# Performance work log

Measured on AMD Instinct MI355X. Metric: run time of the kernel, lower is better.

## Reference

```python
import jax, jax.numpy as jnp
import numpy as np

N, C, OUT, E, H = 4096, 256, 256, 131072, 8
DH = C // H
EPS = 1e-5


def layer_norm(h, g, b):
    mu = jnp.mean(h, axis=-1, keepdims=True)
    var = jnp.mean(jnp.square(h - mu), axis=-1, keepdims=True)
    return (h - mu) * jax.lax.rsqrt(var + EPS) * g + b


def setup_inputs() -> dict:
    key = jax.random.key(0)
    ks = jax.random.split(key, 12)
    s = 1.0 / np.sqrt(C)
    return {
        "x": jax.random.normal(ks[0], (N, C), jnp.float32),
        "edge_index": jax.random.randint(ks[1], (2, E), 0, N, jnp.int32),
        "edge_attr": jax.random.normal(ks[2], (E, C), jnp.float32),
        # nn.MultiheadAttention params
        "in_proj_w": jax.random.uniform(ks[3], (3 * C, C), jnp.float32, -s, s),
        "in_proj_b": jnp.zeros((3 * C,), jnp.float32),
        "attn_out_w": jax.random.uniform(ks[4], (C, C), jnp.float32, -s, s),
        "attn_out_b": jnp.zeros((C,), jnp.float32),
        # edge_mlp: Linear(3C -> OUT) + LayerNorm(OUT)
        "edge_w": jax.random.uniform(ks[5], (OUT, 3 * C), jnp.float32, -1 / np.sqrt(3 * C), 1 / np.sqrt(3 * C)),
        "edge_b": jax.random.uniform(ks[6], (OUT,), jnp.float32, -1 / np.sqrt(3 * C), 1 / np.sqrt(3 * C)),
        "ln1_g": jnp.ones((OUT,), jnp.float32),
        "ln1_b": jnp.zeros((OUT,), jnp.float32),
        # output_proj: Linear(C + OUT -> OUT)
        "out_w": jax.random.uniform(ks[7], (OUT, C + OUT), jnp.float32, -1 / np.sqrt(C + OUT), 1 / np.sqrt(C + OUT)),
        "out_b": jax.random.uniform(ks[8], (OUT,), jnp.float32, -1 / np.sqrt(C + OUT), 1 / np.sqrt(C + OUT)),
        "ln2_g": jnp.ones((OUT,), jnp.float32),
        "ln2_b": jnp.zeros((OUT,), jnp.float32),
    }


def reference(x, edge_index, edge_attr, in_proj_w, in_proj_b, attn_out_w, attn_out_b,
              edge_w, edge_b, ln1_g, ln1_b, out_w, out_b, ln2_g, ln2_b):
    num_nodes = x.shape[0]
    # --- dense self-attention over all nodes (seq len = N, batch 1) ---
    qkv = x @ in_proj_w.T + in_proj_b            # [N, 3C]
    q, k, v = jnp.split(qkv, 3, axis=-1)
    q = q.reshape(num_nodes, H, DH).transpose(1, 0, 2)  # [H, N, DH]
    k = k.reshape(num_nodes, H, DH).transpose(1, 0, 2)
    v = v.reshape(num_nodes, H, DH).transpose(1, 0, 2)
    scores = jnp.einsum("hqd,hkd->hqk", q, k) / np.sqrt(DH)
    attn = jax.nn.softmax(scores, axis=-1)       # dropout inactive at eval
    ctx = jnp.einsum("hqk,hkd->hqd", attn, v)    # [H, N, DH]
    ctx = ctx.transpose(1, 0, 2).reshape(num_nodes, C)
    x_attn = ctx @ attn_out_w.T + attn_out_b     # [N, C]
    # --- vectorized edge messages: gather -> MLP -> scatter-add ---
    row, col = edge_index[0], edge_index[1]
    msg_in = jnp.concatenate([x[row], x[col], edge_attr], axis=-1)  # [E, 3C]
    msg = jax.nn.relu(layer_norm(msg_in @ edge_w.T + edge_b, ln1_g, ln1_b))
    node_messages = jax.ops.segment_sum(msg, col, num_segments=num_nodes)  # [N, OUT]
    # --- combine, project, residual, norm ---
    combined = jnp.concatenate([x_attn, node_messages], axis=-1)
    out = combined @ out_w.T + out_b
    out = out + x                                # OUT == C so residual fires
    return layer_norm(out, ln2_g, ln2_b)
```

## Files before the change

### kernel.cpp

```cpp
#include <hip/hip_runtime.h>
#include <hip/hip_bf16.h>
#include <math.h>

typedef __bf16 bf16;
typedef __bf16 bf16x8 __attribute__((ext_vector_type(8)));
typedef __bf16 bf16x4 __attribute__((ext_vector_type(4)));
typedef float f32x4 __attribute__((ext_vector_type(4)));
typedef float f32x16 __attribute__((ext_vector_type(16)));

#define MFMA16(a, b, c) __builtin_amdgcn_mfma_f32_16x16x32_bf16((a), (b), (c), 0, 0, 0)
#define MFMA32(a, b, c) __builtin_amdgcn_mfma_f32_32x32x16_bf16((a), (b), (c), 0, 0, 0)

#define N_NODES 4096
#define C_DIM   256
#define E_EDGES 131072
#define APAD    280
#define TPAD    260

__device__ __forceinline__ float ldf(const void* p, int i, bool f32) {
    return f32 ? ((const float*)p)[i] : (float)((const bf16*)p)[i];
}

__device__ __forceinline__ bf16x8 ld8(const void* base, size_t off, bool f32) {
    if (f32) {
        const float* p = (const float*)base + off;
        float4 a = *(const float4*)p;
        float4 b = *(const float4*)(p + 4);
        bf16x8 r;
        r[0] = (bf16)a.x; r[1] = (bf16)a.y; r[2] = (bf16)a.z; r[3] = (bf16)a.w;
        r[4] = (bf16)b.x; r[5] = (bf16)b.y; r[6] = (bf16)b.z; r[7] = (bf16)b.w;
        return r;
    }
    return *(const bf16x8*)((const bf16*)base + off);
}

__device__ __forceinline__ unsigned cvtpk(float a, float b) {
    unsigned r;
    asm("v_cvt_pk_bf16_f32 %0, %1, %2" : "=v"(r) : "v"(a), "v"(b));
    return r;
}
__device__ __forceinline__ void pl32swap(unsigned &a, unsigned &b) {
    asm volatile("v_permlane32_swap_b32 %0, %1" : "+v"(a), "+v"(b));
}

union PW { unsigned u[4]; bf16x8 v; };

__global__ __launch_bounds__(64) void detect_dtype(const void* x, int* flag)
{
    const bf16* xb = (const bf16*)x;
    int tid = threadIdx.x;
    int bad = 0;
    for (int i = tid; i < 4096; i += 64) {
        float v = fabsf((float)xb[i]);
        if (!(v >= 1e-6f && v <= 100.0f)) bad++;
    }
#pragma unroll
    for (int m = 1; m < 64; m <<= 1) bad += __shfl_xor(bad, m);
    if (tid == 0) *flag = (bad > 400) ? 1 : 0;
}

__global__ __launch_bounds__(256) void convert_inputs(
    const void* s0, const void* s1, const void* s2, const void* s3, const void* s4,
    bf16* dst, const int* flag)
{
    int idx = blockIdx.x * 256 + threadIdx.x;
    const void* src; int local;
    if (idx < 1048576)      { src = s0; local = idx; }
    else if (idx < 1245184) { src = s1; local = idx - 1048576; }
    else if (idx < 1310720) { src = s2; local = idx - 1245184; }
    else if (idx < 1507328) { src = s3; local = idx - 1310720; }
    else                    { src = s4; local = idx - 1507328; }
    if (*flag) dst[idx] = (bf16)(((const float*)src)[local]);
    else ((unsigned short*)dst)[idx] = ((const unsigned short*)src)[local];
}

__global__ __launch_bounds__(256) void edge_hist(
    const int* __restrict__ ecol, int* __restrict__ counts)
{
    int e = blockIdx.x * 256 + threadIdx.x;
    atomicAdd(&counts[ecol[e]], 1);
}

__global__ __launch_bounds__(256) void edge_scan(
    const int* __restrict__ counts, int* __restrict__ offsets,
    int* __restrict__ cursor)
{
    __shared__ int part[256];
    __shared__ int pref[257];
    int t = threadIdx.x;
    int base = t * 16;
    int s = 0;
#pragma unroll
    for (int i = 0; i < 16; ++i) s += counts[base + i];
    part[t] = s;
    __syncthreads();
    if (t == 0) {
        int run = 0;
        for (int i = 0; i < 256; ++i) { pref[i] = run; run += part[i]; }
        pref[256] = run;
    }
    __syncthreads();
    int off = pref[t];
#pragma unroll
    for (int i = 0; i < 16; ++i) {
        offsets[base + i] = off;
        cursor[base + i]  = off;
        off += counts[base + i];
    }
    if (t == 255) offsets[4096] = off;
}

__global__ __launch_bounds__(256) void edge_scatter(
    const int* __restrict__ ecol, int* __restrict__ cursor,
    int* __restrict__ eid, int* __restrict__ epos)
{
    int e = blockIdx.x * 256 + threadIdx.x;
    int pos = atomicAdd(&cursor[ecol[e]], 1);
    eid[pos] = e;
    epos[e] = pos;
}

__global__ __launch_bounds__(256) void gemm_bt(
    const bf16* __restrict__ A, int lda,
    const bf16* __restrict__ W, int ldw,
    const void* __restrict__ bias,
    void* __restrict__ Cout, int ldc, int c_f32,
    const bf16* __restrict__ resid, int ldr,
    int K, const int* __restrict__ flag)
{
    const bool f32 = (*flag != 0);
    const int wave = threadIdx.x >> 6;
    const int lane = threadIdx.x & 63;
    const int quad = lane >> 4;
    const int l16  = lane & 15;
    const int m_base = blockIdx.x * 32;
    const int n_base = blockIdx.y * 256 + wave * 64;

    const bf16* a0p = A + (size_t)(m_base + l16) * lda + quad * 8;
    const bf16* a1p = a0p + (size_t)16 * lda;
    const bf16* wp  = W + (size_t)(n_base + l16) * ldw + quad * 8;

    f32x4 acc[2][4] = {};
    for (int k = 0; k < K; k += 32) {
        bf16x8 a0 = *(const bf16x8*)(a0p + k);
        bf16x8 a1 = *(const bf16x8*)(a1p + k);
#pragma unroll
        for (int nt = 0; nt < 4; ++nt) {
            bf16x8 b = *(const bf16x8*)(wp + (size_t)nt * 16 * ldw + k);
            acc[0][nt] = MFMA16(a0, b, acc[0][nt]);
            acc[1][nt] = MFMA16(a1, b, acc[1][nt]);
        }
    }
#pragma unroll
    for (int mt = 0; mt < 2; ++mt) {
#pragma unroll
        for (int nt = 0; nt < 4; ++nt) {
            int col = n_base + nt * 16 + l16;
            float bv = bias ? ldf(bias, col, f32) : 0.0f;
#pragma unroll
            for (int r = 0; r < 4; ++r) {
                int row = m_base + mt * 16 + quad * 4 + r;
                float v = acc[mt][nt][r] + bv;
                if (resid) v += (float)resid[(size_t)row * ldr + col];
                if (c_f32) ((float*)Cout)[(size_t)row * ldc + col] = v;
                else       ((bf16*)Cout)[(size_t)row * ldc + col] = (bf16)v;
            }
        }
    }
}

__global__ __launch_bounds__(256) void gemm_uv(
    const bf16* __restrict__ x, const bf16* __restrict__ ew,
    bf16* __restrict__ U, bf16* __restrict__ V)
{
    const int wave = threadIdx.x >> 6;
    const int lane = threadIdx.x & 63;
    const int quad = lane >> 4;
    const int l16  = lane & 15;
    const int m_base = blockIdx.x * 32;
    bf16* dst = blockIdx.y ? V : U;
    const bf16* W = ew + blockIdx.y * 256;

    const bf16* a0p = x + (size_t)(m_base + l16) * 256 + quad * 8;
    const bf16* a1p = a0p + (size_t)16 * 256;
    const bf16* wp  = W + (size_t)(wave * 64 + l16) * 768 + quad * 8;

    f32x4 acc[2][4] = {};
#pragma unroll
    for (int kk = 0; kk < 8; ++kk) {
        int k = kk * 32;
        bf16x8 a0 = *(const bf16x8*)(a0p + k);
        bf16x8 a1 = *(const bf16x8*)(a1p + k);
#pragma unroll
        for (int nt = 0; nt < 4; ++nt) {
            bf16x8 b = *(const bf16x8*)(wp + (size_t)nt * 16 * 768 + k);
            acc[0][nt] = MFMA16(a0, b, acc[0][nt]);
            acc[1][nt] = MFMA16(a1, b, acc[1][nt]);
        }
    }
#pragma unroll
    for (int mt = 0; mt < 2; ++mt)
#pragma unroll
        for (int nt = 0; nt < 4; ++nt) {
            int col = wave * 64 + nt * 16 + l16;
#pragma unroll
            for (int r = 0; r < 4; ++r) {
                int row = m_base + mt * 16 + quad * 4 + r;
                dst[(size_t)row * 256 + col] = (bf16)acc[mt][nt][r];
            }
        }
}

__global__ __launch_bounds__(256) void transpose_v(
    const bf16* __restrict__ qkv, bf16* __restrict__ vt)
{
    __shared__ bf16 t[32][65];
    const int n0 = blockIdx.x * 64;
    const int c0 = blockIdx.y * 32;
    const int tid = threadIdx.x;
    {
        int cl = tid & 31, nl = tid >> 5;
#pragma unroll
        for (int p = 0; p < 8; ++p) {
            int n = nl + p * 8;
            t[cl][n] = qkv[(size_t)(n0 + n) * 768 + 512 + c0 + cl];
        }
    }
    __syncthreads();
    {
        int nn = tid & 63, cc = tid >> 6;
#pragma unroll
        for (int p = 0; p < 8; ++p) {
            int c = cc + p * 4;
            vt[(size_t)(c0 + c) * 4096 + n0 + nn] = t[c][nn];
        }
    }
}

__global__ __launch_bounds__(256) void attn_kernel(
    const bf16* __restrict__ qkv,
    const bf16* __restrict__ vt,
    bf16* __restrict__ ctx)
{
    __shared__ float oL[4][32][33];
    __shared__ float mS[4][32];
    __shared__ float lS[4][32];
    const int tid  = threadIdx.x;
    const int wave = tid >> 6;
    const int lane = tid & 63;
    const int l32  = lane & 31;
    const int hl   = lane >> 5;
    const int h  = blockIdx.x >> 7;
    const int qt = blockIdx.x & 127;

    const float csc = 1.4426950408889634f * 0.17677669529663687f;

    const bf16* qrow = qkv + (size_t)(qt * 32 + l32) * 768 + h * 32 + hl * 8;
    bf16x8 qf1 = *(const bf16x8*)qrow;
    bf16x8 qf2 = *(const bf16x8*)(qrow + 16);

    const bf16* kbp = qkv + 256 + h * 32 + hl * 8;
    const bf16* vrp = vt + (size_t)(h * 32 + l32) * 4096 + hl * 8;

    float mrun = -INFINITY, msc = -INFINITY, lacc = 0.f;
    f32x16 oacc = {};
    const f32x16 z16 = {};

    const int kbeg = wave * 1024;
    for (int k0 = kbeg; k0 < kbeg + 1024; k0 += 32) {
        const bf16* kp = kbp + (size_t)(k0 + l32) * 768;
        bf16x8 kf1 = *(const bf16x8*)kp;
        bf16x8 kf2 = *(const bf16x8*)(kp + 16);
        bf16x8 vf1 = *(const bf16x8*)(vrp + k0);
        bf16x8 vf2 = *(const bf16x8*)(vrp + k0 + 16);

        f32x16 s = MFMA32(kf1, qf1, z16);
        s = MFMA32(kf2, qf2, s);

        float a0 = fmaxf(fmaxf(s[0], s[1]), fmaxf(s[2], s[3]));
        float a1 = fmaxf(fmaxf(s[4], s[5]), fmaxf(s[6], s[7]));
        float a2 = fmaxf(fmaxf(s[8], s[9]), fmaxf(s[10], s[11]));
        float a3 = fmaxf(fmaxf(s[12], s[13]), fmaxf(s[14], s[15]));
        float tm = fmaxf(fmaxf(a0, a1), fmaxf(a2, a3));
        tm = fmaxf(tm, __shfl_xor(tm, 32));

        if (__any(tm > mrun)) {
            float nm = fmaxf(mrun, tm);
            float nmsc = nm * csc;
            float al = exp2f(msc - nmsc);
            mrun = nm; msc = nmsc;
            lacc *= al;
#pragma unroll
            for (int i = 0; i < 16; ++i) oacc[i] *= al;
        }

        float p[16];
#pragma unroll
        for (int i = 0; i < 16; ++i) {
            p[i] = exp2f(__builtin_fmaf(s[i], csc, -msc));
            lacc += p[i];
        }

        unsigned w0 = cvtpk(p[0], p[1]),  w1 = cvtpk(p[2], p[3]);
        unsigned w2 = cvtpk(p[4], p[5]),  w3 = cvtpk(p[6], p[7]);
        unsigned w4 = cvtpk(p[8], p[9]),  w5 = cvtpk(p[10], p[11]);
        unsigned w6 = cvtpk(p[12], p[13]), w7 = cvtpk(p[14], p[15]);
        pl32swap(w0, w2); pl32swap(w1, w3);
        pl32swap(w4, w6); pl32swap(w5, w7);
        PW f1; f1.u[0] = w0; f1.u[1] = w1; f1.u[2] = w2; f1.u[3] = w3;
        PW f2; f2.u[0] = w4; f2.u[1] = w5; f2.u[2] = w6; f2.u[3] = w7;

        oacc = MFMA32(vf1, f1.v, oacc);
        oacc = MFMA32(vf2, f2.v, oacc);
    }

    lacc += __shfl_xor(lacc, 32);
    if (hl == 0) { mS[wave][l32] = mrun; lS[wave][l32] = lacc; }
#pragma unroll
    for (int i = 0; i < 16; ++i) {
        int d = (i & 3) + 8 * (i >> 2) + 4 * hl;
        oL[wave][l32][d] = oacc[i];
    }
    __syncthreads();
    {
        int q = tid >> 3, d0 = (tid & 7) * 4;
        float m0 = mS[0][q], m1 = mS[1][q], m2 = mS[2][q], m3 = mS[3][q];
        float ms = fmaxf(fmaxf(m0, m1), fmaxf(m2, m3));
        float f0 = exp2f((m0 - ms) * csc), f1 = exp2f((m1 - ms) * csc);
        float f2 = exp2f((m2 - ms) * csc), f3 = exp2f((m3 - ms) * csc);
        float ls = lS[0][q] * f0 + lS[1][q] * f1 + lS[2][q] * f2 + lS[3][q] * f3;
        float inv = 1.0f / ls;
        bf16x4 o4;
#pragma unroll
        for (int i = 0; i < 4; ++i) {
            int d = d0 + i;
            float v = (oL[0][q][d] * f0 + oL[1][q][d] * f1 +
                       oL[2][q][d] * f2 + oL[3][q][d] * f3) * inv;
            o4[i] = (bf16)v;
        }
        *(bf16x4*)(ctx + (size_t)(qt * 32 + q) * 256 + h * 32 + d0) = o4;
    }
}

__global__ __launch_bounds__(256) void edge_gemm(
    const void* __restrict__ eattr,
    const bf16* __restrict__ ew,
    const void* __restrict__ eb,
    const int* __restrict__ epos,
    bf16* __restrict__ msgpre, const int* __restrict__ flag)
{
    __shared__ char smem[64 * APAD * 2];
    bf16* Asm = (bf16*)smem;
    float (*Trow)[TPAD] = (float(*)[TPAD])smem;

    const bool f32 = (*flag != 0);
    const int tid  = threadIdx.x;
    const int wave = tid >> 6;
    const int lane = tid & 63;
    const int quad = lane >> 4;
    const int l16  = lane & 15;
    const int e_base = blockIdx.x * 64;

    bf16x8 breg[8][4];
#pragma unroll
    for (int k0 = 0; k0 < 8; ++k0)
#pragma unroll
        for (int nt = 0; nt < 4; ++nt)
            breg[k0][nt] = *(const bf16x8*)(ew +
                (size_t)(wave * 64 + nt * 16 + l16) * 768 + 512 + k0 * 32 + quad * 8);

    {
        int row   = tid >> 2;
        int cbase = (tid & 3) * 64;
        bf16* dst = Asm + row * APAD + cbase;
        if (!f32) {
            const bf16* src = (const bf16*)eattr + (size_t)(e_base + row) * 256 + cbase;
#pragma unroll
            for (int j = 0; j < 8; ++j)
                *(bf16x8*)(dst + j * 8) = *(const bf16x8*)(src + j * 8);
        } else {
            const float* src = (const float*)eattr + (size_t)(e_base + row) * 256 + cbase;
#pragma unroll
            for (int j = 0; j < 8; ++j) {
                float4 a = *(const float4*)(src + j * 8);
                float4 b = *(const float4*)(src + j * 8 + 4);
                bf16x8 r;
                r[0] = (bf16)a.x; r[1] = (bf16)a.y; r[2] = (bf16)a.z; r[3] = (bf16)a.w;
                r[4] = (bf16)b.x; r[5] = (bf16)b.y; r[6] = (bf16)b.z; r[7] = (bf16)b.w;
                *(bf16x8*)(dst + j * 8) = r;
            }
        }
    }
    __syncthreads();

    f32x4 acc[4][4] = {};
#pragma unroll
    for (int k0 = 0; k0 < 8; ++k0) {
#pragma unroll
        for (int mt = 0; mt < 4; ++mt) {
            bf16x8 af = *(const bf16x8*)(Asm + (mt * 16 + l16) * APAD + k0 * 32 + quad * 8);
#pragma unroll
            for (int nt = 0; nt < 4; ++nt)
                acc[mt][nt] = MFMA16(af, breg[k0][nt], acc[mt][nt]);
        }
    }

    float ebv[4];
#pragma unroll
    for (int nt = 0; nt < 4; ++nt)
        ebv[nt] = ldf(eb, wave * 64 + nt * 16 + l16, f32);

    for (int p = 0; p < 2; ++p) {
        __syncthreads();
#pragma unroll
        for (int mtl = 0; mtl < 2; ++mtl) {
            int mt = p * 2 + mtl;
#pragma unroll
            for (int nt = 0; nt < 4; ++nt)
#pragma unroll
                for (int r = 0; r < 4; ++r)
                    Trow[mtl * 16 + quad * 4 + r][wave * 64 + nt * 16 + l16] =
                        acc[mt][nt][r] + ebv[nt];
        }
        __syncthreads();
        {
            int row = tid >> 3;
            int seg = tid & 7;
            int ep = epos[e_base + p * 32 + row];
            const float* tr = &Trow[row][seg * 32];
            bf16* op = msgpre + (size_t)ep * 256 + seg * 32;
#pragma unroll
            for (int i = 0; i < 4; ++i) {
                float4 a = *(const float4*)(tr + i * 8);
                float4 b = *(const float4*)(tr + i * 8 + 4);
                bf16x8 o;
                o[0] = (bf16)a.x; o[1] = (bf16)a.y; o[2] = (bf16)a.z; o[3] = (bf16)a.w;
                o[4] = (bf16)b.x; o[5] = (bf16)b.y; o[6] = (bf16)b.z; o[7] = (bf16)b.w;
                *(bf16x8*)(op + i * 8) = o;
            }
        }
    }
}

__global__ __launch_bounds__(256) void node_ln(
    const bf16* __restrict__ msgpre,
    const int* __restrict__ offsets, const int* __restrict__ eid,
    const int* __restrict__ erow,
    const bf16* __restrict__ U, const bf16* __restrict__ V,
    const void* __restrict__ g1, const void* __restrict__ b1,
    bf16* __restrict__ combined, const int* __restrict__ flag)
{
    __shared__ float accL[4][256];
    const bool f32 = (*flag != 0);
    const int wave = threadIdx.x >> 6;
    const int lane = threadIdx.x & 63;
    const int node = blockIdx.x;
    const int start = offsets[node];
    const int cnt   = offsets[node + 1] - start;

    float glv[4], blv[4], vv[4];
#pragma unroll
    for (int i = 0; i < 4; ++i) {
        glv[i] = ldf(g1, lane * 4 + i, f32);
        blv[i] = ldf(b1, lane * 4 + i, f32);
    }
    {
        bf16x4 v4 = *(const bf16x4*)(V + (size_t)node * 256 + lane * 4);
#pragma unroll
        for (int i = 0; i < 4; ++i) vv[i] = (float)v4[i];
    }

    float nacc[4] = {0.f, 0.f, 0.f, 0.f};
    for (int i = wave; i < cnt; i += 4) {
        int pos = start + i;
        int er = erow[eid[pos]];
        bf16x4 t4 = *(const bf16x4*)(msgpre + (size_t)pos * 256 + lane * 4);
        bf16x4 u4 = *(const bf16x4*)(U + (size_t)er * 256 + lane * 4);
        float val[4];
        float s = 0.f, q = 0.f;
#pragma unroll
        for (int j = 0; j < 4; ++j) {
            val[j] = (float)t4[j] + (float)u4[j] + vv[j];
            s += val[j];
            q = __builtin_fmaf(val[j], val[j], q);
        }
#pragma unroll
        for (int msk = 1; msk < 64; msk <<= 1) {
            s += __shfl_xor(s, msk);
            q += __shfl_xor(q, msk);
        }
        float mean = s * (1.0f / 256.0f);
        float var  = q * (1.0f / 256.0f) - mean * mean;
        float rstd = rsqrtf(var + 1e-5f);
#pragma unroll
        for (int j = 0; j < 4; ++j)
            nacc[j] += fmaxf((val[j] - mean) * rstd * glv[j] + blv[j], 0.0f);
    }
#pragma unroll
    for (int j = 0; j < 4; ++j) accL[wave][lane * 4 + j] = nacc[j];
    __syncthreads();
    if (wave == 0) {
        bf16x4 o4;
#pragma unroll
        for (int j = 0; j < 4; ++j) {
            int c = lane * 4 + j;
            float s = (accL[0][c] + accL[1][c]) + (accL[2][c] + accL[3][c]);
            o4[j] = (bf16)s;
        }
        *(bf16x4*)(combined + (size_t)node * 512 + 256 + lane * 4) = o4;
    }
}

__global__ __launch_bounds__(256) void edge_node(
    const bf16* __restrict__ x,
    const int* __restrict__ erow,
    const void* __restrict__ eattr,
    const bf16* __restrict__ ew,
    const void* __restrict__ eb,
    const void* __restrict__ g1, const void* __restrict__ b1,
    const int* __restrict__ offsets, const int* __restrict__ eid,
    bf16* __restrict__ combined, const int* __restrict__ flag)
{
    __shared__ float part[32][4][2];
    const bool f32 = (*flag != 0);
    const int wave = threadIdx.x >> 6;
    const int lane = threadIdx.x & 63;
    const int quad = lane >> 4;
    const int l16  = lane & 15;
    const int n = blockIdx.x;
    const int start = offsets[n];
    const int cnt   = offsets[n + 1] - start;

    float gv[4], bv[4], ebv[4];
#pragma unroll
    for (int nt = 0; nt < 4; ++nt) {
        int col = wave * 64 + nt * 16 + l16;
        gv[nt]  = ldf(g1, col, f32);
        bv[nt]  = ldf(b1, col, f32);
        ebv[nt] = ldf(eb, col, f32);
    }
    const bf16* wp = ew + (size_t)(wave * 64 + l16) * 768 + quad * 8;
    const bf16* xn = x + (size_t)n * 256 + quad * 8;

    f32x4 acc1[4] = {};
#pragma unroll
    for (int kk = 0; kk < 8; ++kk) {
        bf16x8 a = *(const bf16x8*)(xn + kk * 32);
#pragma unroll
        for (int nt = 0; nt < 4; ++nt) {
            bf16x8 b = *(const bf16x8*)(wp + (size_t)nt * 16 * 768 + 256 + kk * 32);
            acc1[nt] = MFMA16(a, b, acc1[nt]);
        }
    }
    float nacc[4] = {0.f, 0.f, 0.f, 0.f};
    for (int c0 = 0; c0 < cnt; c0 += 32) {
        int i0 = c0 + l16;      i0 = (i0 < cnt) ? i0 : 0;
        int i1 = c0 + 16 + l16; i1 = (i1 < cnt) ? i1 : 0;
        int e0 = eid[start + i0];
        int e1 = eid[start + i1];
        const bf16* xr0 = x + (size_t)erow[e0] * 256 + quad * 8;
        const bf16* xr1 = x + (size_t)erow[e1] * 256 + quad * 8;
        f32x4 acc[2][4];
#pragma unroll
        for (int nt = 0; nt < 4; ++nt) { acc[0][nt] = acc1[nt]; acc[1][nt] = acc1[nt]; }
#pragma unroll
        for (int kk = 0; kk < 8; ++kk) {
            bf16x8 a0 = *(const bf16x8*)(xr0 + kk * 32);
            bf16x8 a1 = *(const bf16x8*)(xr1 + kk * 32);
#pragma unroll
            for (int nt = 0; nt < 4; ++nt) {
                bf16x8 b = *(const bf16x8*)(wp + (size_t)nt * 16 * 768 + kk * 32);
                acc[0][nt] = MFMA16(a0, b, acc[0][nt]);
                acc[1][nt] = MFMA16(a1, b, acc[1][nt]);
            }
        }
#pragma unroll
        for (int kk = 0; kk < 8; ++kk) {
            int koff = quad * 8 + kk * 32;
            bf16x8 a0 = ld8(eattr, (size_t)e0 * 256 + koff, f32);
            bf16x8 a1 = ld8(eattr, (size_t)e1 * 256 + koff, f32);
#pragma unroll
            for (int nt = 0; nt < 4; ++nt) {
                bf16x8 b = *(const bf16x8*)(wp + (size_t)nt * 16 * 768 + 512 + kk * 32);
                acc[0][nt] = MFMA16(a0, b, acc[0][nt]);
                acc[1][nt] = MFMA16(a1, b, acc[1][nt]);
            }
        }
#pragma unroll
        for (int mt = 0; mt < 2; ++mt)
#pragma unroll
            for (int nt = 0; nt < 4; ++nt)
#pragma unroll
                for (int r = 0; r < 4; ++r) acc[mt][nt][r] += ebv[nt];
        float ps[2][4], pq[2][4];
#pragma unroll
        for (int mt = 0; mt < 2; ++mt)
#pragma unroll
            for (int r = 0; r < 4; ++r) {
                float s = 0.f, q = 0.f;
#pragma unroll
                for (int nt = 0; nt < 4; ++nt) {
                    float v = acc[mt][nt][r];
                    s += v; q += v * v;
                }
                ps[mt][r] = s; pq[mt][r] = q;
            }
#pragma unroll
        for (int msk = 1; msk < 16; msk <<= 1)
#pragma unroll
            for (int mt = 0; mt < 2; ++mt)
#pragma unroll
                for (int r = 0; r < 4; ++r) {
                    ps[mt][r] += __shfl_xor(ps[mt][r], msk);
                    pq[mt][r] += __shfl_xor(pq[mt][r], msk);
                }
        if (l16 == 0) {
#pragma unroll
            for (int mt = 0; mt < 2; ++mt)
#pragma unroll
                for (int r = 0; r < 4; ++r) {
                    part[mt * 16 + quad * 4 + r][wave][0] = ps[mt][r];
                    part[mt * 16 + quad * 4 + r][wave][1] = pq[mt][r];
                }
        }
        __syncthreads();
#pragma unroll
        for (int mt = 0; mt < 2; ++mt)
#pragma unroll
            for (int r = 0; r < 4; ++r) {
                int row = mt * 16 + quad * 4 + r;
                float s = part[row][0][0] + part[row][1][0] + part[row][2][0] + part[row][3][0];
                float q = part[row][0][1] + part[row][1][1] + part[row][2][1] + part[row][3][1];
                float mean = s * (1.0f / 256.0f);
                float var  = q * (1.0f / 256.0f) - mean * mean;
                float rstd = rsqrtf(var + 1e-5f);
                if ((c0 + row) < cnt) {
#pragma unroll
                    for (int nt = 0; nt < 4; ++nt) {
                        float val = (acc[mt][nt][r] - mean) * rstd * gv[nt] + bv[nt];
                        nacc[nt] += fmaxf(val, 0.0f);
                    }
                }
            }
        __syncthreads();
    }
#pragma unroll
    for (int nt = 0; nt < 4; ++nt) {
        nacc[nt] += __shfl_xor(nacc[nt], 16);
        nacc[nt] += __shfl_xor(nacc[nt], 32);
    }
    if (quad == 0) {
#pragma unroll
        for (int nt = 0; nt < 4; ++nt)
            combined[(size_t)n * 512 + 256 + wave * 64 + nt * 16 + l16] = (bf16)nacc[nt];
    }
}

__global__ __launch_bounds__(256) void gemm_ln(
    const bf16* __restrict__ A,
    const bf16* __restrict__ W,
    const void* __restrict__ bias,
    const bf16* __restrict__ resid,
    const void* __restrict__ g, const void* __restrict__ bb,
    void* __restrict__ out, const int* __restrict__ flag)
{
    __shared__ float stats[16][4][2];
    const bool f32 = (*flag != 0);
    const int wave = threadIdx.x >> 6;
    const int lane = threadIdx.x & 63;
    const int quad = lane >> 4;
    const int l16  = lane & 15;
    const int m_base = blockIdx.x * 16;

    const bf16* ap = A + (size_t)(m_base + l16) * 512 + quad * 8;
    const bf16* wp = W + (size_t)(wave * 64 + l16) * 512 + quad * 8;

    f32x4 acc[4] = {};
#pragma unroll
    for (int kk = 0; kk < 16; ++kk) {
        int k = kk * 32;
        bf16x8 a = *(const bf16x8*)(ap + k);
#pragma unroll
        for (int nt = 0; nt < 4; ++nt) {
            bf16x8 b = *(const bf16x8*)(wp + (size_t)nt * 16 * 512 + k);
            acc[nt] = MFMA16(a, b, acc[nt]);
        }
    }
    float s[4] = {}, q[4] = {};
#pragma unroll
    for (int nt = 0; nt < 4; ++nt) {
        int col = wave * 64 + nt * 16 + l16;
        float bv = ldf(bias, col, f32);
#pragma unroll
        for (int r = 0; r < 4; ++r) {
            int row = m_base + quad * 4 + r;
            float v = acc[nt][r] + bv + (float)resid[(size_t)row * 256 + col];
            acc[nt][r] = v;
            s[r] += v;
            q[r] = __builtin_fmaf(v, v, q[r]);
        }
    }
#pragma unroll
    for (int msk = 1; msk < 16; msk <<= 1)
#pragma unroll
        for (int r = 0; r < 4; ++r) {
            s[r] += __shfl_xor(s[r], msk);
            q[r] += __shfl_xor(q[r], msk);
        }
    if (l16 == 0) {
#pragma unroll
        for (int r = 0; r < 4; ++r) {
            stats[quad * 4 + r][wave][0] = s[r];
            stats[quad * 4 + r][wave][1] = q[r];
        }
    }
    __syncthreads();
#pragma unroll
    for (int r = 0; r < 4; ++r) {
        int row16 = quad * 4 + r;
        float ss = (stats[row16][0][0] + stats[row16][1][0]) +
                   (stats[row16][2][0] + stats[row16][3][0]);
        float qq = (stats[row16][0][1] + stats[row16][1][1]) +
                   (stats[row16][2][1] + stats[row16][3][1]);
        float mean = ss * (1.0f / 256.0f);
        float var  = qq * (1.0f / 256.0f) - mean * mean;
        float rstd = rsqrtf(var + 1e-5f);
        int row = m_base + row16;
#pragma unroll
        for (int nt = 0; nt < 4; ++nt) {
            int col = wave * 64 + nt * 16 + l16;
            float o = (acc[nt][r] - mean) * rstd * ldf(g, col, f32) + ldf(bb, col, f32);
            if (f32) ((float*)out)[(size_t)row * 256 + col] = o;
            else     ((bf16*)out)[(size_t)row * 256 + col] = (bf16)o;
        }
    }
}

extern "C" void kernel_launch(void* const* d_in, const int* in_sizes, int n_in,
                              void* d_out, int out_size, void* d_ws, size_t ws_size,
                              hipStream_t stream)
{
    const void* x_raw  = d_in[0];
    const int*  eidx   = (const int*)d_in[1];
    const void* eattr  = d_in[2];
    const void* in_w   = d_in[3];
    const void* in_b   = d_in[4];
    const void* ao_w   = d_in[5];
    const void* ao_b   = d_in[6];
    const void* e_w    = d_in[7];
    const void* e_b    = d_in[8];
    const void* g1     = d_in[9];
    const void* b1     = d_in[10];
    const void* o_w    = d_in[11];
    const void* o_b    = d_in[12];
    const void* g2     = d_in[13];
    const void* b2     = d_in[14];

    char* ws = (char*)d_ws;
    bf16*  qkv      = (bf16*)(ws);
    bf16*  vt       = (bf16*)(ws + 6291456);
    bf16*  ctx      = (bf16*)(ws + 8388608);
    bf16*  combined = (bf16*)(ws + 10485760);
    int*   counts   = (int*)(ws + 14680064);
    int*   offsets  = (int*)(ws + 14696448);
    int*   cursor   = (int*)(ws + 14712848);
    int*   eid      = (int*)(ws + 14729232);
    int*   epos     = (int*)(ws + 15253520);
    bf16*  U        = (bf16*)(ws + 18874368);
    bf16*  V        = (bf16*)(ws + 20971520);
    bf16*  canon    = (bf16*)(ws + 23068672);
    int*   flag     = (int*)(ws + 26345472);
    bf16*  msgpre   = (bf16*)(ws + 26345728);

    const size_t WS_NEEDED = 93454592;

    bf16* x_bf   = canon;
    bf16* inw_bf = canon + 1048576;
    bf16* aow_bf = canon + 1245184;
    bf16* ew_bf  = canon + 1310720;
    bf16* ow_bf  = canon + 1507328;

    const int* erow = eidx;
    const int* ecol = eidx + E_EDGES;

    detect_dtype<<<dim3(1), 64, 0, stream>>>(x_raw, flag);
    convert_inputs<<<dim3(6400), 256, 0, stream>>>(x_raw, in_w, ao_w, e_w, o_w,
                                                   canon, flag);
    hipMemsetAsync(counts, 0, 16384, stream);
    edge_hist<<<dim3(E_EDGES / 256), 256, 0, stream>>>(ecol, counts);
    edge_scan<<<dim3(1), 256, 0, stream>>>(counts, offsets, cursor);
    edge_scatter<<<dim3(E_EDGES / 256), 256, 0, stream>>>(ecol, cursor, eid, epos);

    gemm_uv<<<dim3(128, 2), 256, 0, stream>>>(x_bf, ew_bf, U, V);

    gemm_bt<<<dim3(128, 3), 256, 0, stream>>>(x_bf, 256, inw_bf, 256, in_b,
                                              qkv, 768, 0, nullptr, 0, 256, flag);
    transpose_v<<<dim3(64, 8), 256, 0, stream>>>(qkv, vt);
    attn_kernel<<<dim3(1024), 256, 0, stream>>>(qkv, vt, ctx);
    gemm_bt<<<dim3(128, 1), 256, 0, stream>>>(ctx, 256, aow_bf, 256, ao_b,
                                              combined, 512, 0, nullptr, 0, 256, flag);
    if (ws_size >= WS_NEEDED) {
        edge_gemm<<<dim3(E_EDGES / 64), 256, 0, stream>>>(eattr, ew_bf, e_b,
                                                          epos, msgpre, flag);
        node_ln<<<dim3(N_NODES), 256, 0, stream>>>(msgpre, offsets, eid, erow,
                                                   U, V, g1, b1, combined, flag);
    } else {
        edge_node<<<dim3(N_NODES), 256, 0, stream>>>(x_bf, erow, eattr,
                                                     ew_bf, e_b, g1, b1,
                                                     offsets, eid, combined, flag);
    }
    gemm_ln<<<dim3(256), 256, 0, stream>>>(combined, ow_bf, o_b, x_bf,
                                           g2, b2, d_out, flag);
}
```

Baseline: 466.4 us.

## Swap MFMA operands in edge_gemm to store bf16 output directly from registers

Swaps the A/B operands of the MFMA so each lane holds four consecutive output columns for one edge row. The results can then be converted to packed bf16 and written straight to the permuted msgpre rows, which removes the LDS transpose staging and its two barriers per half. The LDS layout of the A tile gains a 16-byte gap every 128 bytes to reduce bank conflicts, and the bias is loaded as vectors up front. In exchange the global stores become 8-byte scattered writes rather than 16-byte coalesced row writes, which may lower store efficiency.

```diff
diff --git a/kernel.cpp b/kernel.cpp
--- a/kernel.cpp
+++ b/kernel.cpp
@@ -15,7 +15,6 @@
 #define C_DIM   256
 #define E_EDGES 131072
 #define APAD    280
-#define TPAD    260
 
 __device__ __forceinline__ float ldf(const void* p, int i, bool f32) {
     return f32 ? ((const float*)p)[i] : (float)((const bf16*)p)[i];
@@ -349,10 +348,7 @@
     const int* __restrict__ epos,
     bf16* __restrict__ msgpre, const int* __restrict__ flag)
 {
-    __shared__ char smem[64 * APAD * 2];
-    bf16* Asm = (bf16*)smem;
-    float (*Trow)[TPAD] = (float(*)[TPAD])smem;
-
+    __shared__ bf16 Asm[64 * APAD];
     const bool f32 = (*flag != 0);
     const int tid  = threadIdx.x;
     const int wave = tid >> 6;
@@ -369,17 +365,31 @@
             breg[k0][nt] = *(const bf16x8*)(ew +
                 (size_t)(wave * 64 + nt * 16 + l16) * 768 + 512 + k0 * 32 + quad * 8);
 
+    float ebv[4][4];
+#pragma unroll
+    for (int nt = 0; nt < 4; ++nt) {
+        int c0 = wave * 64 + nt * 16 + quad * 4;
+        if (f32) {
+            float4 t = *(const float4*)((const float*)eb + c0);
+            ebv[nt][0] = t.x; ebv[nt][1] = t.y; ebv[nt][2] = t.z; ebv[nt][3] = t.w;
+        } else {
+            bf16x4 t = *(const bf16x4*)((const bf16*)eb + c0);
+#pragma unroll
+            for (int j = 0; j < 4; ++j) ebv[nt][j] = (float)t[j];
+        }
+    }
+
     {
         int row   = tid >> 2;
-        int cbase = (tid & 3) * 64;
-        bf16* dst = Asm + row * APAD + cbase;
+        int chunk = tid & 3;
+        char* dstb = (char*)Asm + row * (APAD * 2) + chunk * 144;
         if (!f32) {
-            const bf16* src = (const bf16*)eattr + (size_t)(e_base + row) * 256 + cbase;
+            const bf16* src = (const bf16*)eattr + (size_t)(e_base + row) * 256 + chunk * 64;
 #pragma unroll
             for (int j = 0; j < 8; ++j)
-                *(bf16x8*)(dst + j * 8) = *(const bf16x8*)(src + j * 8);
+                *(bf16x8*)(dstb + j * 16) = *(const bf16x8*)(src + j * 8);
         } else {
-            const float* src = (const float*)eattr + (size_t)(e_base + row) * 256 + cbase;
+            const float* src = (const float*)eattr + (size_t)(e_base + row) * 256 + chunk * 64;
 #pragma unroll
             for (int j = 0; j < 8; ++j) {
                 float4 a = *(const float4*)(src + j * 8);
@@ -387,7 +397,7 @@
                 bf16x8 r;
                 r[0] = (bf16)a.x; r[1] = (bf16)a.y; r[2] = (bf16)a.z; r[3] = (bf16)a.w;
                 r[4] = (bf16)b.x; r[5] = (bf16)b.y; r[6] = (bf16)b.z; r[7] = (bf16)b.w;
-                *(bf16x8*)(dst + j * 8) = r;
+                *(bf16x8*)(dstb + j * 16) = r;
             }
         }
     }
@@ -396,48 +406,27 @@
     f32x4 acc[4][4] = {};
 #pragma unroll
     for (int k0 = 0; k0 < 8; ++k0) {
+        const int koff = k0 * 64 + ((k0 >> 1) << 4);
 #pragma unroll
         for (int mt = 0; mt < 4; ++mt) {
-            bf16x8 af = *(const bf16x8*)(Asm + (mt * 16 + l16) * APAD + k0 * 32 + quad * 8);
+            const char* arow = (const char*)Asm + (mt * 16 + l16) * (APAD * 2);
+            bf16x8 af = *(const bf16x8*)(arow + koff + (quad << 4));
 #pragma unroll
             for (int nt = 0; nt < 4; ++nt)
-                acc[mt][nt] = MFMA16(af, breg[k0][nt], acc[mt][nt]);
-        }
-    }
-
-    float ebv[4];
-#pragma unroll
-    for (int nt = 0; nt < 4; ++nt)
-        ebv[nt] = ldf(eb, wave * 64 + nt * 16 + l16, f32);
-
-    for (int p = 0; p < 2; ++p) {
-        __syncthreads();
-#pragma unroll
-        for (int mtl = 0; mtl < 2; ++mtl) {
-            int mt = p * 2 + mtl;
-#pragma unroll
-            for (int nt = 0; nt < 4; ++nt)
-#pragma unroll
-                for (int r = 0; r < 4; ++r)
-                    Trow[mtl * 16 + quad * 4 + r][wave * 64 + nt * 16 + l16] =
-                        acc[mt][nt][r] + ebv[nt];
-        }
-        __syncthreads();
-        {
-            int row = tid >> 3;
-            int seg = tid & 7;
-            int ep = epos[e_base + p * 32 + row];
-            const float* tr = &Trow[row][seg * 32];
-            bf16* op = msgpre + (size_t)ep * 256 + seg * 32;
-#pragma unroll
-            for (int i = 0; i < 4; ++i) {
-                float4 a = *(const float4*)(tr + i * 8);
-                float4 b = *(const float4*)(tr + i * 8 + 4);
-                bf16x8 o;
-                o[0] = (bf16)a.x; o[1] = (bf16)a.y; o[2] = (bf16)a.z; o[3] = (bf16)a.w;
-                o[4] = (bf16)b.x; o[5] = (bf16)b.y; o[6] = (bf16)b.z; o[7] = (bf16)b.w;
-                *(bf16x8*)(op + i * 8) = o;
-            }
+                acc[mt][nt] = MFMA16(breg[k0][nt], af, acc[mt][nt]);
+        }
+    }
+
+#pragma unroll
+    for (int mt = 0; mt < 4; ++mt) {
+        int ep = epos[e_base + mt * 16 + l16];
+        bf16* op = msgpre + (size_t)ep * 256 + wave * 64 + quad * 4;
+#pragma unroll
+        for (int nt = 0; nt < 4; ++nt) {
+            unsigned d0 = cvtpk(acc[mt][nt][0] + ebv[nt][0], acc[mt][nt][1] + ebv[nt][1]);
+            unsigned d1 = cvtpk(acc[mt][nt][2] + ebv[nt][2], acc[mt][nt][3] + ebv[nt][3]);
+            uint2 st; st.x = d0; st.y = d1;
+            *(uint2*)(op + nt * 16) = st;
         }
     }
 }
```

Result: slower. 483.0 us (+3.6%).
